# Kernel optimization log

Measured on AMD Instinct MI355X. Metric: run time of the kernel, lower is better.

## Reference

```python
import jax, jax.numpy as jnp
import numpy as np

N_NODES = 50000
N_EDGES = 800000
IN_C, HID_C, OUT_C = 128, 128, 64


def setup_inputs() -> dict:
    key = jax.random.key(0)
    ks = jax.random.split(key, 8)
    x = jax.random.normal(ks[0], (N_NODES, IN_C), dtype=jnp.float32)
    edge_index = jax.random.randint(ks[1], (2, N_EDGES), 0, N_NODES, dtype=jnp.int32)
    edge_weight = jax.random.uniform(ks[2], (N_EDGES,), dtype=jnp.float32)
    node_type = jax.random.randint(ks[3], (N_NODES,), 0, 4, dtype=jnp.int32)
    s1 = 1.0 / np.sqrt(IN_C)
    s2 = 1.0 / np.sqrt(HID_C)
    return {
        "x": x,
        "edge_index": edge_index,
        "edge_weight": edge_weight,
        "node_type": node_type,
        "W_l1": jax.random.normal(ks[4], (HID_C, IN_C), dtype=jnp.float32) * s1,
        "b_l1": jnp.zeros((HID_C,), dtype=jnp.float32),
        "W_r1": jax.random.normal(ks[5], (HID_C, IN_C), dtype=jnp.float32) * s1,
        "W_l2": jax.random.normal(ks[6], (OUT_C, HID_C), dtype=jnp.float32) * s2,
        "b_l2": jnp.zeros((OUT_C,), dtype=jnp.float32),
        "W_r2": jax.random.normal(ks[7], (OUT_C, HID_C), dtype=jnp.float32) * s2,
    }


def _sage_conv(h, src, dst, edge_weight, W_l, b_l, W_r, num_nodes):
    # message: edge_weight * x_src, mean-aggregated at dst (PyG SAGEConv mean aggr)
    msg = h[src] * edge_weight[:, None]                                  # [E, C]
    agg = jax.ops.segment_sum(msg, dst, num_segments=num_nodes)          # [N, C]
    deg = jax.ops.segment_sum(jnp.ones_like(edge_weight), dst, num_segments=num_nodes)
    agg = agg / jnp.maximum(deg, 1.0)[:, None]
    # out = lin_l(agg) + lin_r(root); bias only on lin_l (PyG convention)
    return agg @ W_l.T + b_l + h @ W_r.T


def reference(x, edge_index, edge_weight, node_type, W_l1, b_l1, W_r1, W_l2, b_l2, W_r2):
    num_nodes = x.shape[0]
    src, dst = edge_index[0], edge_index[1]
    h = _sage_conv(x, src, dst, edge_weight, W_l1, b_l1, W_r1, num_nodes)
    h = jax.nn.relu(h)  # dropout p=0.0 -> identity
    out = _sage_conv(h, src, dst, edge_weight, W_l2, b_l2, W_r2, num_nodes)
    return out
```

## Files before the change

kernel.cpp:

```cpp
#include <hip/hip_runtime.h>

constexpr int IN_C  = 128;
constexpr int HID_C = 128;
constexpr int OUT_C = 64;

constexpr int BSHIFT    = 7;
constexpr int NBUCK_MAX = 512;
constexpr int CAP       = 4096;
constexpr int EPB       = 2048;

typedef short bf16x8 __attribute__((ext_vector_type(8)));
typedef float f32x4  __attribute__((ext_vector_type(4)));
typedef float f32x2  __attribute__((ext_vector_type(2)));

__device__ __forceinline__ unsigned short f2b(float f) {
    unsigned u = __float_as_uint(f);
    unsigned r = (u + 0x7fffu + ((u >> 16) & 1u)) >> 16;
    return (unsigned short)r;
}
__device__ __forceinline__ float b2f_lo(unsigned u) { return __uint_as_float(u << 16); }
__device__ __forceinline__ float b2f_hi(unsigned u) { return __uint_as_float(u & 0xffff0000u); }
__device__ __forceinline__ unsigned char f2fp8(float f) {
    int p = __builtin_amdgcn_cvt_pk_fp8_f32(f, f, 0, false);
    return (unsigned char)(p & 0xff);
}

struct Acc8 {
    float a0 = 0, a1 = 0, a2 = 0, a3 = 0, a4 = 0, a5 = 0, a6 = 0, a7 = 0;
    __device__ __forceinline__ void acc_fp8(uint2 v, float wt) {
        f32x2 p0 = __builtin_amdgcn_cvt_pk_f32_fp8(v.x, false);
        f32x2 p1 = __builtin_amdgcn_cvt_pk_f32_fp8(v.x, true);
        f32x2 p2 = __builtin_amdgcn_cvt_pk_f32_fp8(v.y, false);
        f32x2 p3 = __builtin_amdgcn_cvt_pk_f32_fp8(v.y, true);
        a0 = fmaf(p0[0], wt, a0); a1 = fmaf(p0[1], wt, a1);
        a2 = fmaf(p1[0], wt, a2); a3 = fmaf(p1[1], wt, a3);
        a4 = fmaf(p2[0], wt, a4); a5 = fmaf(p2[1], wt, a5);
        a6 = fmaf(p3[0], wt, a6); a7 = fmaf(p3[1], wt, a7);
    }
    __device__ __forceinline__ void acc_bf16(uint4 v, float wt) {
        a0 = fmaf(b2f_lo(v.x), wt, a0); a1 = fmaf(b2f_hi(v.x), wt, a1);
        a2 = fmaf(b2f_lo(v.y), wt, a2); a3 = fmaf(b2f_hi(v.y), wt, a3);
        a4 = fmaf(b2f_lo(v.z), wt, a4); a5 = fmaf(b2f_hi(v.z), wt, a5);
        a6 = fmaf(b2f_lo(v.w), wt, a6); a7 = fmaf(b2f_hi(v.w), wt, a7);
    }
};


__global__ __launch_bounds__(256) void k_init(
    int* __restrict__ bcnt, int NBUCK,
    const float* __restrict__ wa, const float* __restrict__ wb,
    const float* __restrict__ wc, const float* __restrict__ wd,
    unsigned short* __restrict__ wab, unsigned short* __restrict__ wbb,
    unsigned short* __restrict__ wcb, unsigned short* __restrict__ wdb) {
    if (blockIdx.x == 0) {
        for (int i = threadIdx.x; i < NBUCK; i += 256) bcnt[i] = 0;
        return;
    }
    const int NW1 = HID_C * IN_C, NW3 = OUT_C * HID_C;
    int off = ((blockIdx.x - 1) * 256 + threadIdx.x) * 4;
    if (off >= 2 * NW1 + 2 * NW3) return;
    const float* s; unsigned short* d;
    if (off < NW1) { s = wa; d = wab; }
    else { off -= NW1;
        if (off < NW1) { s = wb; d = wbb; }
        else { off -= NW1;
            if (off < NW3) { s = wc; d = wcb; }
            else { off -= NW3; s = wd; d = wdb; }
        }
    }
    float4 v = *reinterpret_cast<const float4*>(s + off);
    ushort4 o;
    o.x = f2b(v.x); o.y = f2b(v.y); o.z = f2b(v.z); o.w = f2b(v.w);
    *reinterpret_cast<ushort4*>(d + off) = o;
}


template <int K, int CO_M, int CO_R, bool A_F32, bool OM_FP8>
__device__ __forceinline__ void gemm_body(
    int bx, const void* __restrict__ Av, const unsigned short* __restrict__ Wm,
    const unsigned short* __restrict__ Wr, void* __restrict__ Om,
    unsigned short* __restrict__ Or, int N) {
    int wave = threadIdx.x >> 6;
    int lane = threadIdx.x & 63;
    int tile = bx * 4 + wave;
    int m0 = tile * 16;
    if (m0 >= N) return;
    int lm = lane & 15;
    int quad = lane >> 4;
    int row = min(m0 + lm, N - 1);

    bf16x8 afrag[K / 32];
    if (A_F32) {
        const float* A = (const float*)Av;
#pragma unroll
        for (int kk = 0; kk < K / 32; kk++) {
            const float* ap = A + (size_t)row * K + kk * 32 + quad * 8;
            float4 u0 = *reinterpret_cast<const float4*>(ap);
            float4 u1 = *reinterpret_cast<const float4*>(ap + 4);
            bf16x8 a;
            a[0] = (short)f2b(u0.x); a[1] = (short)f2b(u0.y);
            a[2] = (short)f2b(u0.z); a[3] = (short)f2b(u0.w);
            a[4] = (short)f2b(u1.x); a[5] = (short)f2b(u1.y);
            a[6] = (short)f2b(u1.z); a[7] = (short)f2b(u1.w);
            afrag[kk] = a;
        }
    } else {
        const unsigned short* A = (const unsigned short*)Av;
#pragma unroll
        for (int kk = 0; kk < K / 32; kk++)
            afrag[kk] = *reinterpret_cast<const bf16x8*>(A + (size_t)row * K + kk * 32 + quad * 8);
    }

#pragma unroll
    for (int j = 0; j < CO_M / 16; j++) {
        const unsigned short* wrow = Wm + (size_t)(j * 16 + lm) * K + quad * 8;
        f32x4 acc = {0.f, 0.f, 0.f, 0.f};
#pragma unroll
        for (int kk = 0; kk < K / 32; kk++) {
            bf16x8 b = *reinterpret_cast<const bf16x8*>(wrow + kk * 32);
            acc = __builtin_amdgcn_mfma_f32_16x16x32_bf16(afrag[kk], b, acc, 0, 0, 0);
        }
#pragma unroll
        for (int r = 0; r < 4; r++) {
            int node = m0 + quad * 4 + r;
            if (node < N) {
                if (OM_FP8)
                    ((unsigned char*)Om)[(size_t)node * CO_M + j * 16 + lm] = f2fp8(acc[r]);
                else
                    ((unsigned short*)Om)[(size_t)node * CO_M + j * 16 + lm] = f2b(acc[r]);
            }
        }
    }
#pragma unroll
    for (int j = 0; j < CO_R / 16; j++) {
        const unsigned short* wrow = Wr + (size_t)(j * 16 + lm) * K + quad * 8;
        f32x4 acc = {0.f, 0.f, 0.f, 0.f};
#pragma unroll
        for (int kk = 0; kk < K / 32; kk++) {
            bf16x8 b = *reinterpret_cast<const bf16x8*>(wrow + kk * 32);
            acc = __builtin_amdgcn_mfma_f32_16x16x32_bf16(afrag[kk], b, acc, 0, 0, 0);
        }
#pragma unroll
        for (int r = 0; r < 4; r++) {
            int node = m0 + quad * 4 + r;
            if (node < N) Or[(size_t)node * CO_R + j * 16 + lm] = f2b(acc[r]);
        }
    }
}


__global__ __launch_bounds__(256) void k_fill_gemm1(
    const int* __restrict__ src, const int* __restrict__ dst,
    const float* __restrict__ ew, int E, int NBUCK, int EBLK,
    int* __restrict__ bcnt, int2* __restrict__ brec,
    const float* __restrict__ x, const unsigned short* __restrict__ wl1b,
    const unsigned short* __restrict__ wr1b, unsigned char* __restrict__ msg1,
    unsigned short* __restrict__ root, int N) {
    if (blockIdx.x >= EBLK) {
        gemm_body<IN_C, HID_C, HID_C, true, true>(
            blockIdx.x - EBLK, x, wl1b, wr1b, msg1, root, N);
        return;
    }
    __shared__ int lh[NBUCK_MAX], lbase[NBUCK_MAX], lcnt[NBUCK_MAX];
    for (int i = threadIdx.x; i < NBUCK; i += 256) { lh[i] = 0; lcnt[i] = 0; }
    __syncthreads();
    int base = blockIdx.x * EPB;
#pragma unroll
    for (int i = 0; i < EPB / 256; i++) {
        int e = base + i * 256 + threadIdx.x;
        if (e < E) atomicAdd(&lh[dst[e] >> BSHIFT], 1);
    }
    __syncthreads();
    for (int i = threadIdx.x; i < NBUCK; i += 256) {
        int v = lh[i];
        lbase[i] = v ? (i * CAP + atomicAdd(&bcnt[i], v)) : 0;
    }
    __syncthreads();
#pragma unroll
    for (int i = 0; i < EPB / 256; i++) {
        int e = base + i * 256 + threadIdx.x;
        if (e < E) {
            int d = dst[e];
            int b = d >> BSHIFT;
            int loc = atomicAdd(&lcnt[b], 1);
            int2 r;
            r.x = __float_as_int(ew[e]);
            r.y = (src[e] & 0xffff) | ((d & 127) << 16);
            brec[(size_t)lbase[b] + loc] = r;
        }
    }
}

__global__ __launch_bounds__(256) void k_bcsr(const int2* __restrict__ brec,
                                              const int* __restrict__ bcnt, int N,
                                              int2* __restrict__ row_range,
                                              unsigned int* __restrict__ csr) {
    __shared__ int lh[128], lex[128], lcnt[128], sc[128];
    int b = blockIdx.x, t = threadIdx.x;
    if (t < 128) { lh[t] = 0; lcnt[t] = 0; }
    __syncthreads();
    int beg = b * CAP;
    int cnt = bcnt[b];
    for (int e = t; e < cnt; e += 256)
        atomicAdd(&lh[(brec[beg + e].y >> 16) & 127], 1);
    __syncthreads();
    if (t < 128) sc[t] = lh[t];
    __syncthreads();
    for (int d = 1; d < 128; d <<= 1) {
        int v = (t >= d && t < 128) ? sc[t - d] : 0;
        __syncthreads();
        if (t < 128) sc[t] += v;
        __syncthreads();
    }
    if (t < 128) lex[t] = sc[t] - lh[t];
    __syncthreads();
    int node_base = b << BSHIFT;
    if (t < 128 && node_base + t < N)
        row_range[node_base + t] = make_int2(beg + lex[t], beg + sc[t]);
    for (int e = t; e < cnt; e += 256) {
        int2 r = brec[beg + e];
        int d = (r.y >> 16) & 127;
        int loc = atomicAdd(&lcnt[d], 1);
        unsigned int w16 = (unsigned int)f2b(__int_as_float(r.x)) << 16;
        csr[(size_t)beg + lex[d] + loc] = (unsigned int)(r.y & 0xffff) | w16;
    }
}


template <int C, bool RELU, bool OUT_BF, bool MSG_FP8>
__global__ __launch_bounds__(256) void k_combine(
    const void* __restrict__ msgp,
    const unsigned short* __restrict__ root,
    const float* __restrict__ bias,
    const int2* __restrict__ row_range, const unsigned int* __restrict__ crec,
    void* __restrict__ outp, int N) {
    constexpr int LPN = C / 8;
    constexpr int NPB = 256 / LPN;
    int tid = threadIdx.x;
    int node = blockIdx.x * NPB + tid / LPN;
    if (node >= N) return;
    int c8 = (tid % LPN) * 8;
    int2 rr = row_range[node];
    int beg = rr.x, end = rr.y;

    const unsigned char*  m8  = (const unsigned char*)msgp;
    const unsigned short* m16 = (const unsigned short*)msgp;

    Acc8 ac;
    int e = beg;
    for (; e + 3 < end; e += 4) {
        unsigned int r0e = crec[e],     r1e = crec[e + 1];
        unsigned int r2e = crec[e + 2], r3e = crec[e + 3];
        float w0 = b2f_hi(r0e), w1 = b2f_hi(r1e);
        float w2 = b2f_hi(r2e), w3 = b2f_hi(r3e);
        int s0 = r0e & 0xffff, s1 = r1e & 0xffff;
        int s2 = r2e & 0xffff, s3 = r3e & 0xffff;
        if (MSG_FP8) {
            uint2 v0 = *reinterpret_cast<const uint2*>(m8 + (size_t)s0 * C + c8);
            uint2 v1 = *reinterpret_cast<const uint2*>(m8 + (size_t)s1 * C + c8);
            uint2 v2 = *reinterpret_cast<const uint2*>(m8 + (size_t)s2 * C + c8);
            uint2 v3 = *reinterpret_cast<const uint2*>(m8 + (size_t)s3 * C + c8);
            ac.acc_fp8(v0, w0); ac.acc_fp8(v1, w1);
            ac.acc_fp8(v2, w2); ac.acc_fp8(v3, w3);
        } else {
            uint4 v0 = *reinterpret_cast<const uint4*>(m16 + (size_t)s0 * C + c8);
            uint4 v1 = *reinterpret_cast<const uint4*>(m16 + (size_t)s1 * C + c8);
            uint4 v2 = *reinterpret_cast<const uint4*>(m16 + (size_t)s2 * C + c8);
            uint4 v3 = *reinterpret_cast<const uint4*>(m16 + (size_t)s3 * C + c8);
            ac.acc_bf16(v0, w0); ac.acc_bf16(v1, w1);
            ac.acc_bf16(v2, w2); ac.acc_bf16(v3, w3);
        }
    }
    for (; e < end; e++) {
        unsigned int r0e = crec[e];
        float w0 = b2f_hi(r0e);
        int s0 = r0e & 0xffff;
        if (MSG_FP8) {
            uint2 v0 = *reinterpret_cast<const uint2*>(m8 + (size_t)s0 * C + c8);
            ac.acc_fp8(v0, w0);
        } else {
            uint4 v0 = *reinterpret_cast<const uint4*>(m16 + (size_t)s0 * C + c8);
            ac.acc_bf16(v0, w0);
        }
    }
    float inv = 1.0f / fmaxf((float)(end - beg), 1.0f);
    uint4 rv = *reinterpret_cast<const uint4*>(root + (size_t)node * C + c8);
    float4 b0 = *reinterpret_cast<const float4*>(bias + c8);
    float4 b1 = *reinterpret_cast<const float4*>(bias + c8 + 4);
    float o0 = fmaf(ac.a0, inv, b0.x + b2f_lo(rv.x)), o1 = fmaf(ac.a1, inv, b0.y + b2f_hi(rv.x));
    float o2 = fmaf(ac.a2, inv, b0.z + b2f_lo(rv.y)), o3 = fmaf(ac.a3, inv, b0.w + b2f_hi(rv.y));
    float o4 = fmaf(ac.a4, inv, b1.x + b2f_lo(rv.z)), o5 = fmaf(ac.a5, inv, b1.y + b2f_hi(rv.z));
    float o6 = fmaf(ac.a6, inv, b1.z + b2f_lo(rv.w)), o7 = fmaf(ac.a7, inv, b1.w + b2f_hi(rv.w));
    if (RELU) {
        o0 = fmaxf(o0, 0.f); o1 = fmaxf(o1, 0.f); o2 = fmaxf(o2, 0.f); o3 = fmaxf(o3, 0.f);
        o4 = fmaxf(o4, 0.f); o5 = fmaxf(o5, 0.f); o6 = fmaxf(o6, 0.f); o7 = fmaxf(o7, 0.f);
    }
    if (OUT_BF) {
        unsigned short* op = (unsigned short*)outp + (size_t)node * C + c8;
        uint4 pk;
        pk.x = (unsigned)f2b(o0) | ((unsigned)f2b(o1) << 16);
        pk.y = (unsigned)f2b(o2) | ((unsigned)f2b(o3) << 16);
        pk.z = (unsigned)f2b(o4) | ((unsigned)f2b(o5) << 16);
        pk.w = (unsigned)f2b(o6) | ((unsigned)f2b(o7) << 16);
        *reinterpret_cast<uint4*>(op) = pk;
    } else {
        float* op = (float*)outp + (size_t)node * C + c8;
        *reinterpret_cast<float4*>(op)     = make_float4(o0, o1, o2, o3);
        *reinterpret_cast<float4*>(op + 4) = make_float4(o4, o5, o6, o7);
    }
}


template <int K, int CO_M, int CO_R, bool A_F32, bool OM_FP8>
__global__ __launch_bounds__(256) void k_gemm_mfma(
    const void* __restrict__ Av, const unsigned short* __restrict__ Wm,
    const unsigned short* __restrict__ Wr, void* __restrict__ Om,
    unsigned short* __restrict__ Or, int N) {
    gemm_body<K, CO_M, CO_R, A_F32, OM_FP8>(blockIdx.x, Av, Wm, Wr, Om, Or, N);
}


extern "C" void kernel_launch(void* const* d_in, const int* in_sizes, int n_in,
                              void* d_out, int out_size, void* d_ws, size_t ws_size,
                              hipStream_t stream) {
    const float* x    = (const float*)d_in[0];
    const int*   eidx = (const int*)d_in[1];
    const float* ew   = (const float*)d_in[2];
    const float* W_l1 = (const float*)d_in[4];
    const float* b_l1 = (const float*)d_in[5];
    const float* W_r1 = (const float*)d_in[6];
    const float* W_l2 = (const float*)d_in[7];
    const float* b_l2 = (const float*)d_in[8];
    const float* W_r2 = (const float*)d_in[9];
    float* out = (float*)d_out;

    const int N = in_sizes[0] / IN_C;
    const int E = in_sizes[1] / 2;
    const int* src = eidx;
    const int* dst = eidx + E;
    const int NBUCK = (N + 127) >> BSHIFT;
    const int EBLK = (E + EPB - 1) / EPB;
    const int WBLK = ((2 * HID_C * IN_C + 2 * OUT_C * HID_C) / 4 + 255) / 256;

    char* p = (char*)d_ws;
    auto carve = [&](size_t bytes) -> char* {
        char* r = p;
        p += (bytes + 255) & ~(size_t)255;
        return r;
    };
    int*  bcnt      = (int*)carve((size_t)NBUCK * 4);
    int2* row_range = (int2*)carve((size_t)N * 8);
    int2* brec      = (int2*)carve((size_t)NBUCK * CAP * 8);
    unsigned int* csr = (unsigned int*)carve((size_t)NBUCK * CAP * 4);
    unsigned short* wl1b = (unsigned short*)carve((size_t)HID_C * IN_C * 2);
    unsigned short* wr1b = (unsigned short*)carve((size_t)HID_C * IN_C * 2);
    unsigned short* wl2b = (unsigned short*)carve((size_t)OUT_C * HID_C * 2);
    unsigned short* wr2b = (unsigned short*)carve((size_t)OUT_C * HID_C * 2);
    unsigned short* hb   = (unsigned short*)carve((size_t)N * HID_C * 2);
    unsigned char*  msg1 = (unsigned char*)carve((size_t)N * HID_C);
    unsigned short* msg2 = (unsigned short*)carve((size_t)N * OUT_C * 2);
    unsigned short* root = (unsigned short*)carve((size_t)N * HID_C * 2);

    int tiles = (N + 15) / 16;
    int gblk = (tiles + 3) / 4;

    k_init<<<1 + WBLK, 256, 0, stream>>>(bcnt, NBUCK,
        W_l1, W_r1, W_l2, W_r2, wl1b, wr1b, wl2b, wr2b);
    k_fill_gemm1<<<EBLK + gblk, 256, 0, stream>>>(
        src, dst, ew, E, NBUCK, EBLK, bcnt, brec,
        x, wl1b, wr1b, msg1, root, N);
    k_bcsr<<<NBUCK, 256, 0, stream>>>(brec, bcnt, N, row_range, csr);
    {
        int npb = 256 / (HID_C / 8);
        k_combine<HID_C, true, true, true><<<(N + npb - 1) / npb, 256, 0, stream>>>(
            msg1, root, b_l1, row_range, csr, hb, N);
    }
    k_gemm_mfma<HID_C, OUT_C, OUT_C, false, false><<<gblk, 256, 0, stream>>>(
        hb, wl2b, wr2b, msg2, root, N);
    {
        int npb = 256 / (OUT_C / 8);
        k_combine<OUT_C, false, false, false><<<(N + npb - 1) / npb, 256, 0, stream>>>(
            msg2, root, b_l2, row_range, csr, out, N);
    }
}
```

Baseline: 198.6 us.

## Fuse layer-1 combine with layer-2 GEMM via shared-memory hidden tile

```diff
diff --git a/kernel.cpp b/kernel.cpp
--- a/kernel.cpp
+++ b/kernel.cpp
@@ -7,7 +7,7 @@
 constexpr int BSHIFT    = 7;
 constexpr int NBUCK_MAX = 512;
 constexpr int CAP       = 4096;
-constexpr int EPB       = 2048;
+constexpr int EPB       = 16384;
 
 typedef short bf16x8 __attribute__((ext_vector_type(8)));
 typedef float f32x4  __attribute__((ext_vector_type(4)));
@@ -75,11 +75,11 @@
 }
 
 
-template <int K, int CO_M, int CO_R, bool A_F32, bool OM_FP8>
-__device__ __forceinline__ void gemm_body(
-    int bx, const void* __restrict__ Av, const unsigned short* __restrict__ Wm,
-    const unsigned short* __restrict__ Wr, void* __restrict__ Om,
+__device__ __forceinline__ void gemm1_body(
+    int bx, const float* __restrict__ A, const unsigned short* __restrict__ Wm,
+    const unsigned short* __restrict__ Wr, unsigned char* __restrict__ Om,
     unsigned short* __restrict__ Or, int N) {
+    constexpr int K = IN_C;
     int wave = threadIdx.x >> 6;
     int lane = threadIdx.x & 63;
     int tile = bx * 4 + wave;
@@ -90,29 +90,20 @@
     int row = min(m0 + lm, N - 1);
 
     bf16x8 afrag[K / 32];
-    if (A_F32) {
-        const float* A = (const float*)Av;
-#pragma unroll
-        for (int kk = 0; kk < K / 32; kk++) {
-            const float* ap = A + (size_t)row * K + kk * 32 + quad * 8;
-            float4 u0 = *reinterpret_cast<const float4*>(ap);
-            float4 u1 = *reinterpret_cast<const float4*>(ap + 4);
-            bf16x8 a;
-            a[0] = (short)f2b(u0.x); a[1] = (short)f2b(u0.y);
-            a[2] = (short)f2b(u0.z); a[3] = (short)f2b(u0.w);
-            a[4] = (short)f2b(u1.x); a[5] = (short)f2b(u1.y);
-            a[6] = (short)f2b(u1.z); a[7] = (short)f2b(u1.w);
-            afrag[kk] = a;
-        }
-    } else {
-        const unsigned short* A = (const unsigned short*)Av;
-#pragma unroll
-        for (int kk = 0; kk < K / 32; kk++)
-            afrag[kk] = *reinterpret_cast<const bf16x8*>(A + (size_t)row * K + kk * 32 + quad * 8);
-    }
-
-#pragma unroll
-    for (int j = 0; j < CO_M / 16; j++) {
+#pragma unroll
+    for (int kk = 0; kk < K / 32; kk++) {
+        const float* ap = A + (size_t)row * K + kk * 32 + quad * 8;
+        float4 u0 = *reinterpret_cast<const float4*>(ap);
+        float4 u1 = *reinterpret_cast<const float4*>(ap + 4);
+        bf16x8 a;
+        a[0] = (short)f2b(u0.x); a[1] = (short)f2b(u0.y);
+        a[2] = (short)f2b(u0.z); a[3] = (short)f2b(u0.w);
+        a[4] = (short)f2b(u1.x); a[5] = (short)f2b(u1.y);
+        a[6] = (short)f2b(u1.z); a[7] = (short)f2b(u1.w);
+        afrag[kk] = a;
+    }
+#pragma unroll
+    for (int j = 0; j < HID_C / 16; j++) {
         const unsigned short* wrow = Wm + (size_t)(j * 16 + lm) * K + quad * 8;
         f32x4 acc = {0.f, 0.f, 0.f, 0.f};
 #pragma unroll
@@ -123,16 +114,11 @@
 #pragma unroll
         for (int r = 0; r < 4; r++) {
             int node = m0 + quad * 4 + r;
-            if (node < N) {
-                if (OM_FP8)
-                    ((unsigned char*)Om)[(size_t)node * CO_M + j * 16 + lm] = f2fp8(acc[r]);
-                else
-                    ((unsigned short*)Om)[(size_t)node * CO_M + j * 16 + lm] = f2b(acc[r]);
-            }
-        }
-    }
-#pragma unroll
-    for (int j = 0; j < CO_R / 16; j++) {
+            if (node < N) Om[(size_t)node * HID_C + j * 16 + lm] = f2fp8(acc[r]);
+        }
+    }
+#pragma unroll
+    for (int j = 0; j < HID_C / 16; j++) {
         const unsigned short* wrow = Wr + (size_t)(j * 16 + lm) * K + quad * 8;
         f32x4 acc = {0.f, 0.f, 0.f, 0.f};
 #pragma unroll
@@ -143,7 +129,7 @@
 #pragma unroll
         for (int r = 0; r < 4; r++) {
             int node = m0 + quad * 4 + r;
-            if (node < N) Or[(size_t)node * CO_R + j * 16 + lm] = f2b(acc[r]);
+            if (node < N) Or[(size_t)node * HID_C + j * 16 + lm] = f2b(acc[r]);
         }
     }
 }
@@ -155,17 +141,16 @@
     int* __restrict__ bcnt, int2* __restrict__ brec,
     const float* __restrict__ x, const unsigned short* __restrict__ wl1b,
     const unsigned short* __restrict__ wr1b, unsigned char* __restrict__ msg1,
-    unsigned short* __restrict__ root, int N) {
+    unsigned short* __restrict__ root1, int N) {
     if (blockIdx.x >= EBLK) {
-        gemm_body<IN_C, HID_C, HID_C, true, true>(
-            blockIdx.x - EBLK, x, wl1b, wr1b, msg1, root, N);
+        gemm1_body(blockIdx.x - EBLK, x, wl1b, wr1b, msg1, root1, N);
         return;
     }
     __shared__ int lh[NBUCK_MAX], lbase[NBUCK_MAX], lcnt[NBUCK_MAX];
     for (int i = threadIdx.x; i < NBUCK; i += 256) { lh[i] = 0; lcnt[i] = 0; }
     __syncthreads();
     int base = blockIdx.x * EPB;
-#pragma unroll
+#pragma unroll 4
     for (int i = 0; i < EPB / 256; i++) {
         int e = base + i * 256 + threadIdx.x;
         if (e < E) atomicAdd(&lh[dst[e] >> BSHIFT], 1);
@@ -176,7 +161,7 @@
         lbase[i] = v ? (i * CAP + atomicAdd(&bcnt[i], v)) : 0;
     }
     __syncthreads();
-#pragma unroll
+#pragma unroll 4
     for (int i = 0; i < EPB / 256; i++) {
         int e = base + i * 256 + threadIdx.x;
         if (e < E) {
@@ -227,13 +212,109 @@
 }
 
 
-template <int C, bool RELU, bool OUT_BF, bool MSG_FP8>
-__global__ __launch_bounds__(256) void k_combine(
-    const void* __restrict__ msgp,
-    const unsigned short* __restrict__ root,
+constexpr int HSTRIDE = HID_C + 8;
+
+__global__ __launch_bounds__(256) void k_comb1_gemm2(
+    const unsigned char* __restrict__ msg1,
+    const unsigned short* __restrict__ root1,
+    const float* __restrict__ b1,
+    const int2* __restrict__ row_range, const unsigned int* __restrict__ crec,
+    const unsigned short* __restrict__ wl2b,
+    const unsigned short* __restrict__ wr2b,
+    unsigned short* __restrict__ msg2,
+    unsigned short* __restrict__ root2,
+    int N) {
+    __shared__ unsigned short hls[16 * HSTRIDE];
+    int tid = threadIdx.x;
+    int nl = tid >> 4;
+    int m0 = blockIdx.x * 16;
+    int node = m0 + nl;
+    int c8 = (tid & 15) * 8;
+    bool valid = node < N;
+
+    int beg = 0, end = 0;
+    if (valid) { int2 rr = row_range[node]; beg = rr.x; end = rr.y; }
+
+    Acc8 ac;
+    int e = beg;
+    for (; e + 3 < end; e += 4) {
+        unsigned int r0e = crec[e],     r1e = crec[e + 1];
+        unsigned int r2e = crec[e + 2], r3e = crec[e + 3];
+        float w0 = b2f_hi(r0e), w1 = b2f_hi(r1e);
+        float w2 = b2f_hi(r2e), w3 = b2f_hi(r3e);
+        uint2 v0 = *reinterpret_cast<const uint2*>(msg1 + (size_t)(r0e & 0xffff) * HID_C + c8);
+        uint2 v1 = *reinterpret_cast<const uint2*>(msg1 + (size_t)(r1e & 0xffff) * HID_C + c8);
+        uint2 v2 = *reinterpret_cast<const uint2*>(msg1 + (size_t)(r2e & 0xffff) * HID_C + c8);
+        uint2 v3 = *reinterpret_cast<const uint2*>(msg1 + (size_t)(r3e & 0xffff) * HID_C + c8);
+        ac.acc_fp8(v0, w0); ac.acc_fp8(v1, w1);
+        ac.acc_fp8(v2, w2); ac.acc_fp8(v3, w3);
+    }
+    for (; e < end; e++) {
+        unsigned int r0e = crec[e];
+        uint2 v0 = *reinterpret_cast<const uint2*>(msg1 + (size_t)(r0e & 0xffff) * HID_C + c8);
+        ac.acc_fp8(v0, b2f_hi(r0e));
+    }
+    uint4 pk = {0, 0, 0, 0};
+    if (valid) {
+        float inv = 1.0f / fmaxf((float)(end - beg), 1.0f);
+        uint4 rv = *reinterpret_cast<const uint4*>(root1 + (size_t)node * HID_C + c8);
+        float4 b0 = *reinterpret_cast<const float4*>(b1 + c8);
+        float4 b1v = *reinterpret_cast<const float4*>(b1 + c8 + 4);
+        float o0 = fmaxf(fmaf(ac.a0, inv, b0.x + b2f_lo(rv.x)), 0.f);
+        float o1 = fmaxf(fmaf(ac.a1, inv, b0.y + b2f_hi(rv.x)), 0.f);
+        float o2 = fmaxf(fmaf(ac.a2, inv, b0.z + b2f_lo(rv.y)), 0.f);
+        float o3 = fmaxf(fmaf(ac.a3, inv, b0.w + b2f_hi(rv.y)), 0.f);
+        float o4 = fmaxf(fmaf(ac.a4, inv, b1v.x + b2f_lo(rv.z)), 0.f);
+        float o5 = fmaxf(fmaf(ac.a5, inv, b1v.y + b2f_hi(rv.z)), 0.f);
+        float o6 = fmaxf(fmaf(ac.a6, inv, b1v.z + b2f_lo(rv.w)), 0.f);
+        float o7 = fmaxf(fmaf(ac.a7, inv, b1v.w + b2f_hi(rv.w)), 0.f);
+        pk.x = (unsigned)f2b(o0) | ((unsigned)f2b(o1) << 16);
+        pk.y = (unsigned)f2b(o2) | ((unsigned)f2b(o3) << 16);
+        pk.z = (unsigned)f2b(o4) | ((unsigned)f2b(o5) << 16);
+        pk.w = (unsigned)f2b(o6) | ((unsigned)f2b(o7) << 16);
+    }
+    *reinterpret_cast<uint4*>(&hls[nl * HSTRIDE + c8]) = pk;
+    __syncthreads();
+
+    int wave = tid >> 6;
+    int lane = tid & 63;
+    int lm = lane & 15;
+    int quad = lane >> 4;
+
+    bf16x8 afrag[4];
+#pragma unroll
+    for (int kk = 0; kk < 4; kk++)
+        afrag[kk] = *reinterpret_cast<const bf16x8*>(&hls[lm * HSTRIDE + kk * 32 + quad * 8]);
+
+#pragma unroll
+    for (int t = 0; t < 2; t++) {
+        int jt = wave * 2 + t;
+        const unsigned short* W = (jt < 4) ? wl2b : wr2b;
+        unsigned short* O = (jt < 4) ? msg2 : root2;
+        int j = jt & 3;
+        const unsigned short* wrow = W + (size_t)(j * 16 + lm) * HID_C + quad * 8;
+        f32x4 acc = {0.f, 0.f, 0.f, 0.f};
+#pragma unroll
+        for (int kk = 0; kk < 4; kk++) {
+            bf16x8 b = *reinterpret_cast<const bf16x8*>(wrow + kk * 32);
+            acc = __builtin_amdgcn_mfma_f32_16x16x32_bf16(afrag[kk], b, acc, 0, 0, 0);
+        }
+#pragma unroll
+        for (int r = 0; r < 4; r++) {
+            int nd = m0 + quad * 4 + r;
+            if (nd < N) O[(size_t)nd * OUT_C + j * 16 + lm] = f2b(acc[r]);
+        }
+    }
+}
+
+
+__global__ __launch_bounds__(256) void k_combine2(
+    const unsigned short* __restrict__ msg2,
+    const unsigned short* __restrict__ root2,
     const float* __restrict__ bias,
     const int2* __restrict__ row_range, const unsigned int* __restrict__ crec,
-    void* __restrict__ outp, int N) {
+    float* __restrict__ out, int N) {
+    constexpr int C = OUT_C;
     constexpr int LPN = C / 8;
     constexpr int NPB = 256 / LPN;
     int tid = threadIdx.x;
@@ -243,80 +324,34 @@
     int2 rr = row_range[node];
     int beg = rr.x, end = rr.y;
 
-    const unsigned char*  m8  = (const unsigned char*)msgp;
-    const unsigned short* m16 = (const unsigned short*)msgp;
-
     Acc8 ac;
     int e = beg;
     for (; e + 3 < end; e += 4) {
         unsigned int r0e = crec[e],     r1e = crec[e + 1];
         unsigned int r2e = crec[e + 2], r3e = crec[e + 3];
-        float w0 = b2f_hi(r0e), w1 = b2f_hi(r1e);
-        float w2 = b2f_hi(r2e), w3 = b2f_hi(r3e);
-        int s0 = r0e & 0xffff, s1 = r1e & 0xffff;
-        int s2 = r2e & 0xffff, s3 = r3e & 0xffff;
-        if (MSG_FP8) {
-            uint2 v0 = *reinterpret_cast<const uint2*>(m8 + (size_t)s0 * C + c8);
-            uint2 v1 = *reinterpret_cast<const uint2*>(m8 + (size_t)s1 * C + c8);
-            uint2 v2 = *reinterpret_cast<const uint2*>(m8 + (size_t)s2 * C + c8);
-            uint2 v3 = *reinterpret_cast<const uint2*>(m8 + (size_t)s3 * C + c8);
-            ac.acc_fp8(v0, w0); ac.acc_fp8(v1, w1);
-            ac.acc_fp8(v2, w2); ac.acc_fp8(v3, w3);
-        } else {
-            uint4 v0 = *reinterpret_cast<const uint4*>(m16 + (size_t)s0 * C + c8);
-            uint4 v1 = *reinterpret_cast<const uint4*>(m16 + (size_t)s1 * C + c8);
-            uint4 v2 = *reinterpret_cast<const uint4*>(m16 + (size_t)s2 * C + c8);
-            uint4 v3 = *reinterpret_cast<const uint4*>(m16 + (size_t)s3 * C + c8);
-            ac.acc_bf16(v0, w0); ac.acc_bf16(v1, w1);
-            ac.acc_bf16(v2, w2); ac.acc_bf16(v3, w3);
-        }
+        uint4 v0 = *reinterpret_cast<const uint4*>(msg2 + (size_t)(r0e & 0xffff) * C + c8);
+        uint4 v1 = *reinterpret_cast<const uint4*>(msg2 + (size_t)(r1e & 0xffff) * C + c8);
+        uint4 v2 = *reinterpret_cast<const uint4*>(msg2 + (size_t)(r2e & 0xffff) * C + c8);
+        uint4 v3 = *reinterpret_cast<const uint4*>(msg2 + (size_t)(r3e & 0xffff) * C + c8);
+        ac.acc_bf16(v0, b2f_hi(r0e)); ac.acc_bf16(v1, b2f_hi(r1e));
+        ac.acc_bf16(v2, b2f_hi(r2e)); ac.acc_bf16(v3, b2f_hi(r3e));
     }
     for (; e < end; e++) {
         unsigned int r0e = crec[e];
-        float w0 = b2f_hi(r0e);
-        int s0 = r0e & 0xffff;
-        if (MSG_FP8) {
-            uint2 v0 = *reinterpret_cast<const uint2*>(m8 + (size_t)s0 * C + c8);
-            ac.acc_fp8(v0, w0);
-        } else {
-            uint4 v0 = *reinterpret_cast<const uint4*>(m16 + (size_t)s0 * C + c8);
-            ac.acc_bf16(v0, w0);
-        }
+        uint4 v0 = *reinterpret_cast<const uint4*>(msg2 + (size_t)(r0e & 0xffff) * C + c8);
+        ac.acc_bf16(v0, b2f_hi(r0e));
     }
     float inv = 1.0f / fmaxf((float)(end - beg), 1.0f);
-    uint4 rv = *reinterpret_cast<const uint4*>(root + (size_t)node * C + c8);
+    uint4 rv = *reinterpret_cast<const uint4*>(root2 + (size_t)node * C + c8);
     float4 b0 = *reinterpret_cast<const float4*>(bias + c8);
     float4 b1 = *reinterpret_cast<const float4*>(bias + c8 + 4);
-    float o0 = fmaf(ac.a0, inv, b0.x + b2f_lo(rv.x)), o1 = fmaf(ac.a1, inv, b0.y + b2f_hi(rv.x));
-    float o2 = fmaf(ac.a2, inv, b0.z + b2f_lo(rv.y)), o3 = fmaf(ac.a3, inv, b0.w + b2f_hi(rv.y));
-    float o4 = fmaf(ac.a4, inv, b1.x + b2f_lo(rv.z)), o5 = fmaf(ac.a5, inv, b1.y + b2f_hi(rv.z));
-    float o6 = fmaf(ac.a6, inv, b1.z + b2f_lo(rv.w)), o7 = fmaf(ac.a7, inv, b1.w + b2f_hi(rv.w));
-    if (RELU) {
-        o0 = fmaxf(o0, 0.f); o1 = fmaxf(o1, 0.f); o2 = fmaxf(o2, 0.f); o3 = fmaxf(o3, 0.f);
-        o4 = fmaxf(o4, 0.f); o5 = fmaxf(o5, 0.f); o6 = fmaxf(o6, 0.f); o7 = fmaxf(o7, 0.f);
-    }
-    if (OUT_BF) {
-        unsigned short* op = (unsigned short*)outp + (size_t)node * C + c8;
-        uint4 pk;
-        pk.x = (unsigned)f2b(o0) | ((unsigned)f2b(o1) << 16);
-        pk.y = (unsigned)f2b(o2) | ((unsigned)f2b(o3) << 16);
-        pk.z = (unsigned)f2b(o4) | ((unsigned)f2b(o5) << 16);
-        pk.w = (unsigned)f2b(o6) | ((unsigned)f2b(o7) << 16);
-        *reinterpret_cast<uint4*>(op) = pk;
-    } else {
-        float* op = (float*)outp + (size_t)node * C + c8;
-        *reinterpret_cast<float4*>(op)     = make_float4(o0, o1, o2, o3);
-        *reinterpret_cast<float4*>(op + 4) = make_float4(o4, o5, o6, o7);
-    }
-}
-
-
-template <int K, int CO_M, int CO_R, bool A_F32, bool OM_FP8>
-__global__ __launch_bounds__(256) void k_gemm_mfma(
-    const void* __restrict__ Av, const unsigned short* __restrict__ Wm,
-    const unsigned short* __restrict__ Wr, void* __restrict__ Om,
-    unsigned short* __restrict__ Or, int N) {
-    gemm_body<K, CO_M, CO_R, A_F32, OM_FP8>(blockIdx.x, Av, Wm, Wr, Om, Or, N);
+    float* op = out + (size_t)node * C + c8;
+    *reinterpret_cast<float4*>(op) = make_float4(
+        fmaf(ac.a0, inv, b0.x + b2f_lo(rv.x)), fmaf(ac.a1, inv, b0.y + b2f_hi(rv.x)),
+        fmaf(ac.a2, inv, b0.z + b2f_lo(rv.y)), fmaf(ac.a3, inv, b0.w + b2f_hi(rv.y)));
+    *reinterpret_cast<float4*>(op + 4) = make_float4(
+        fmaf(ac.a4, inv, b1.x + b2f_lo(rv.z)), fmaf(ac.a5, inv, b1.y + b2f_hi(rv.z)),
+        fmaf(ac.a6, inv, b1.z + b2f_lo(rv.w)), fmaf(ac.a7, inv, b1.w + b2f_hi(rv.w)));
 }
 
 
@@ -356,10 +391,10 @@
     unsigned short* wr1b = (unsigned short*)carve((size_t)HID_C * IN_C * 2);
     unsigned short* wl2b = (unsigned short*)carve((size_t)OUT_C * HID_C * 2);
     unsigned short* wr2b = (unsigned short*)carve((size_t)OUT_C * HID_C * 2);
-    unsigned short* hb   = (unsigned short*)carve((size_t)N * HID_C * 2);
     unsigned char*  msg1 = (unsigned char*)carve((size_t)N * HID_C);
+    unsigned short* root1 = (unsigned short*)carve((size_t)N * HID_C * 2);
     unsigned short* msg2 = (unsigned short*)carve((size_t)N * OUT_C * 2);
-    unsigned short* root = (unsigned short*)carve((size_t)N * HID_C * 2);
+    unsigned short* root2 = (unsigned short*)carve((size_t)N * OUT_C * 2);
 
     int tiles = (N + 15) / 16;
     int gblk = (tiles + 3) / 4;
@@ -368,18 +403,10 @@
         W_l1, W_r1, W_l2, W_r2, wl1b, wr1b, wl2b, wr2b);
     k_fill_gemm1<<<EBLK + gblk, 256, 0, stream>>>(
         src, dst, ew, E, NBUCK, EBLK, bcnt, brec,
-        x, wl1b, wr1b, msg1, root, N);
+        x, wl1b, wr1b, msg1, root1, N);
     k_bcsr<<<NBUCK, 256, 0, stream>>>(brec, bcnt, N, row_range, csr);
-    {
-        int npb = 256 / (HID_C / 8);
-        k_combine<HID_C, true, true, true><<<(N + npb - 1) / npb, 256, 0, stream>>>(
-            msg1, root, b_l1, row_range, csr, hb, N);
-    }
-    k_gemm_mfma<HID_C, OUT_C, OUT_C, false, false><<<gblk, 256, 0, stream>>>(
-        hb, wl2b, wr2b, msg2, root, N);
-    {
-        int npb = 256 / (OUT_C / 8);
-        k_combine<OUT_C, false, false, false><<<(N + npb - 1) / npb, 256, 0, stream>>>(
-            msg2, root, b_l2, row_range, csr, out, N);
-    }
-}
+    k_comb1_gemm2<<<tiles, 256, 0, stream>>>(
+        msg1, root1, b_l1, row_range, csr, wl2b, wr2b, msg2, root2, N);
+    k_combine2<<<(N + 31) / 32, 256, 0, stream>>>(
+        msg2, root2, b_l2, row_range, csr, out, N);
+}
```

Result: slower. 216.8 us (+9.2%).
